# Kernel optimization log

Measured on AMD Instinct MI355X. Metric: run time of the kernel, lower is better.

## Reference

```python
import jax, jax.numpy as jnp
import numpy as np

DIM = 768  # N, feature length and Linear dim
B, C = 16, 1024  # batch, token count


def setup_inputs() -> dict:
    key = jax.random.key(0)
    ks = jax.random.split(key, 7)
    s = 1.0 / np.sqrt(DIM)
    return {
        "x": jax.random.normal(ks[0], (B, C, DIM), dtype=jnp.float32),
        "Wq": jax.random.uniform(ks[1], (DIM, DIM), jnp.float32, -s, s),
        "bq": jax.random.uniform(ks[2], (DIM,), jnp.float32, -s, s),
        "Wk": jax.random.uniform(ks[3], (DIM, DIM), jnp.float32, -s, s),
        "bk": jax.random.uniform(ks[4], (DIM,), jnp.float32, -s, s),
        "Wv": jax.random.uniform(ks[5], (DIM, DIM), jnp.float32, -s, s),
        "bv": jax.random.uniform(ks[6], (DIM,), jnp.float32, -s, s),
    }


def reference(x, Wq, bq, Wk, bk, Wv, bv):
    # x: [B, C, N] with N == DIM; Linears act on last axis (torch y = x W^T + b)
    Bb, Cc, N = x.shape
    q = jnp.einsum("bcn,dn->bcd", x, Wq) + bq
    k = jnp.einsum("bcn,dn->bcd", x, Wk) + bk
    v = jnp.einsum("bcn,dn->bcd", x, Wv) + bv
    attn = jax.nn.softmax(jnp.einsum("bcd,bed->bce", q, k) * (N ** -0.5), axis=-1)  # [B,C,C]
    out = jnp.einsum("bce,ben->bcn", attn, v)  # [B,C,N]
    # faithful to torch: transpose(1,2) then reshape back to (B,C,N) -- a buffer reinterpretation
    out = jnp.transpose(out, (0, 2, 1)).reshape(Bb, Cc, N)
    return out + x  # dropout is identity at inference
```

## Files before the change

kernel.cpp:

```cpp
#include <hip/hip_runtime.h>
#include <hip/hip_bf16.h>

typedef __bf16 v8bf __attribute__((ext_vector_type(8)));
typedef float f32x4 __attribute__((ext_vector_type(4)));

static __device__ __forceinline__ unsigned short f2b(float f){
  union { float f; unsigned int u; } c; c.f = f;
  return (unsigned short)((c.u + 0x7FFFu + ((c.u >> 16) & 1u)) >> 16);
}
static __device__ __forceinline__ float b2f(unsigned int h){
  union { unsigned int u; float f; } c; c.u = h << 16; return c.f;
}

static __device__ __forceinline__ void gld_lds16(const void* g, void* l){
  __builtin_amdgcn_global_load_lds(
      (const __attribute__((address_space(1))) unsigned int*)g,
      (__attribute__((address_space(3))) unsigned int*)l, 16, 0, 0);
}

#define FENCE __builtin_amdgcn_sched_barrier(0)

template<int NW>
static __device__ __forceinline__ void gemm2p(
    const unsigned short* __restrict__ A, int lda,
    const unsigned short* __restrict__ B, int ldb,
    int NT, unsigned short* smem, f32x4 acc[8][NW])
{
  const int tid  = threadIdx.x;
  const int lane = tid & 63;
  const int w    = tid >> 6;
  const int wr   = w >> 2, wc = w & 3;
  const int lr   = lane & 15, lg = lane >> 4;
  char* sm = (char*)smem;
  constexpr int BBUF = NW*8192;

  #pragma unroll
  for (int m=0;m<8;++m)
    #pragma unroll
    for (int n=0;n<NW;++n)
      acc[m][n] = (f32x4){0.f,0.f,0.f,0.f};

  const int rloc = tid >> 3;
  const int scol = ((tid & 7) ^ ((tid >> 3) & 7)) << 3;
  const unsigned short* Ab0 = A + (size_t)rloc*lda + scol;
  const unsigned short* Bb0 = B + (size_t)rloc*ldb + scol;

  auto stA = [&](int ab, int i, int kE){
    gld_lds16(Ab0 + (size_t)(i*64)*lda + kE, sm + ab*32768 + i*8192 + w*1024);
  };
  auto stB = [&](int db, int i, int kE){
    gld_lds16(Bb0 + (size_t)(i*64)*ldb + kE, sm + 98304 + db*BBUF + i*8192 + w*1024);
  };

  const int ce0 = (((lg*8))      ^ ((lr&7)<<3)) * 2;
  const int ce1 = (((32 + lg*8)) ^ ((lr&7)<<3)) * 2;

  v8bf aLo[4][2], aHi[4][2], bE[NW][2], bO[NW][2];

  auto rdAh = [&](v8bf (&dst)[4][2], int ab, int half){
    char* base = sm + ab*32768 + (wr*128 + half*64 + lr)*128;
    #pragma unroll
    for (int f=0; f<4; ++f){
      char* rp = base + f*2048;
      dst[f][0] = *(const v8bf*)(rp + ce0);
      dst[f][1] = *(const v8bf*)(rp + ce1);
    }
  };
  auto rdB = [&](v8bf (&dst)[NW][2], int db){
    char* base = sm + 98304 + db*BBUF + (wc*(NW*16) + lr)*128;
    #pragma unroll
    for (int n=0;n<NW;++n){
      char* rp = base + n*2048;
      dst[n][0] = *(const v8bf*)(rp + ce0);
      dst[n][1] = *(const v8bf*)(rp + ce1);
    }
  };

  auto tile = [&](int kt, v8bf (&bcur)[NW][2], v8bf (&bnext)[NW][2]){
    const int ab_r = kt % 3;
    const int ab_n = (ab_r==2) ? 0 : ab_r+1;
    const int ab_s = (ab_n==2) ? 0 : ab_n+1;
    const int db_r = kt & 1;
    const int kS = (kt+2 < NT ? kt+2 : NT-1)*64;

    stA(ab_s,0,kS); stA(ab_s,1,kS); stA(ab_s,2,kS); stA(ab_s,3,kS);
    rdAh(aHi, ab_r, 1);
    FENCE; asm volatile("s_waitcnt lgkmcnt(8)" ::: "memory"); FENCE;
    __builtin_amdgcn_s_setprio(1);
    #pragma unroll
    for (int f=0; f<4; ++f)
      #pragma unroll
      for (int n=0;n<NW;++n){
        acc[f][n] = __builtin_amdgcn_mfma_f32_16x16x32_bf16(aLo[f][0], bcur[n][0], acc[f][n], 0,0,0);
        acc[f][n] = __builtin_amdgcn_mfma_f32_16x16x32_bf16(aLo[f][1], bcur[n][1], acc[f][n], 0,0,0);
      }
    __builtin_amdgcn_s_setprio(0);
    asm volatile("s_waitcnt vmcnt(4)" ::: "memory");
    __builtin_amdgcn_s_barrier();

    #pragma unroll
    for (int i=0;i<NW;++i) stB(db_r, i, kS);
    rdAh(aLo, ab_n, 0);
    rdB(bnext, db_r^1);
    FENCE; asm volatile("s_waitcnt lgkmcnt(14)" ::: "memory"); FENCE;
    __builtin_amdgcn_s_setprio(1);
    #pragma unroll
    for (int f=0; f<4; ++f)
      #pragma unroll
      for (int n=0;n<NW;++n){
        acc[4+f][n] = __builtin_amdgcn_mfma_f32_16x16x32_bf16(aHi[f][0], bcur[n][0], acc[4+f][n], 0,0,0);
        acc[4+f][n] = __builtin_amdgcn_mfma_f32_16x16x32_bf16(aHi[f][1], bcur[n][1], acc[4+f][n], 0,0,0);
      }
    __builtin_amdgcn_s_setprio(0);
    __builtin_amdgcn_s_barrier();
  };

  #pragma unroll
  for (int i=0;i<4;++i)  stA(0,i,0);
  #pragma unroll
  for (int i=0;i<NW;++i) stB(0,i,0);
  #pragma unroll
  for (int i=0;i<4;++i)  stA(1,i,64);
  #pragma unroll
  for (int i=0;i<NW;++i) stB(1,i,64);
  asm volatile("s_waitcnt vmcnt(7)" ::: "memory");
  __builtin_amdgcn_s_barrier();
  rdAh(aLo, 0, 0);
  rdB(bE, 0);

  for (int kt = 0; kt < NT; kt += 2) {
    tile(kt,   bE, bO);
    tile(kt+1, bO, bE);
  }
}

static __device__ __forceinline__ void gemm256v1(
    const unsigned short* __restrict__ A, int lda,
    const unsigned short* __restrict__ B, int ldb,
    int NT, unsigned short* smem, f32x4 acc[8][4])
{
  const int tid  = threadIdx.x;
  const int lane = tid & 63;
  const int w    = tid >> 6;
  const int wr   = w >> 2, wc = w & 3;
  const int lr   = lane & 15, lg = lane >> 4;
  char* sm = (char*)smem;

  #pragma unroll
  for (int m=0;m<8;++m)
    #pragma unroll
    for (int n=0;n<4;++n)
      acc[m][n] = (f32x4){0.f,0.f,0.f,0.f};

  const int rloc = tid >> 3;
  const int scol = ((tid & 7) ^ ((tid >> 3) & 7)) << 3;
  const unsigned short* Ab0 = A + (size_t)rloc*lda + scol;
  const unsigned short* Bb0 = B + (size_t)rloc*ldb + scol;

  auto stA = [&](int ds, int i, int kE){
    gld_lds16(Ab0 + (size_t)(i*64)*lda + kE, sm + ds*32768 + i*8192 + w*1024);
  };
  auto stB = [&](int ds, int i, int kE){
    gld_lds16(Bb0 + (size_t)(i*64)*ldb + kE, sm + 65536 + ds*32768 + i*8192 + w*1024);
  };

  #pragma unroll
  for (int i=0;i<4;++i) stA(0,i,0);
  #pragma unroll
  for (int i=0;i<4;++i) stB(0,i,0);
  #pragma unroll
  for (int i=0;i<4;++i) stB(1,i,64);
  asm volatile("s_waitcnt vmcnt(4)" ::: "memory");
  __builtin_amdgcn_s_barrier();

  const int ce0 = (((lg*8))      ^ ((lr&7)<<3)) * 2;
  const int ce1 = (((32 + lg*8)) ^ ((lr&7)<<3)) * 2;

  for (int kt = 0; kt < NT; ++kt) {
    const int d  = kt & 1;
    char* Abase = sm + d*32768 + wr*16384;
    char* Bbase = sm + 65536 + d*32768 + wc*8192;
    const int kA = (kt+1 < NT ? kt+1 : NT-1)*64;
    const int kB = (kt+2 < NT ? kt+2 : NT-1)*64;
    v8bf bfr[4][2], af0[2][2], af1[2][2];

    auto rdA = [&](v8bf (&dst)[2][2], int qq){
      #pragma unroll
      for (int mm=0;mm<2;++mm){
        char* rp = Abase + ((qq*2+mm)*16+lr)*128;
        dst[mm][0] = *(const v8bf*)(rp + ce0);
        dst[mm][1] = *(const v8bf*)(rp + ce1);
      }
    };
    auto domfma = [&](v8bf (&cur)[2][2], int qq){
      #pragma unroll
      for (int mm=0;mm<2;++mm)
        #pragma unroll
        for (int n=0;n<4;++n){
          acc[qq*2+mm][n] = __builtin_amdgcn_mfma_f32_16x16x32_bf16(cur[mm][0], bfr[n][0], acc[qq*2+mm][n], 0,0,0);
          acc[qq*2+mm][n] = __builtin_amdgcn_mfma_f32_16x16x32_bf16(cur[mm][1], bfr[n][1], acc[qq*2+mm][n], 0,0,0);
        }
    };

    #pragma unroll
    for (int q=0;q<4;++q) {
      if (q==0) {
        #pragma unroll
        for (int n=0;n<4;++n){
          char* rp = Bbase + (n*16+lr)*128;
          bfr[n][0] = *(const v8bf*)(rp + ce0);
          bfr[n][1] = *(const v8bf*)(rp + ce1);
        }
        rdA(af0, 0);
      } else {
        if ((q&1)==0) rdA(af0, q); else rdA(af1, q);
      }
      if      (q==0){ stA(d^1,0,kA); stA(d^1,1,kA); }
      else if (q==1){ stA(d^1,2,kA); stA(d^1,3,kA); }
      else if (q==2){ stB(d,0,kB);   stB(d,1,kB);   }
      else          { stB(d,2,kB);   stB(d,3,kB);   }
      __builtin_amdgcn_s_barrier();
      asm volatile("s_waitcnt lgkmcnt(0)" ::: "memory");
      FENCE;
      __builtin_amdgcn_s_setprio(1);
      if ((q&1)==0) domfma(af0, q); else domfma(af1, q);
      __builtin_amdgcn_s_setprio(0);
      if (q==3) asm volatile("s_waitcnt vmcnt(4)" ::: "memory");
      __builtin_amdgcn_s_barrier();
    }
  }
}

__global__ __launch_bounds__(256) void convert_kernel(
    const float* __restrict__ x,
    const float* __restrict__ Wq, const float* __restrict__ Wk,
    const float* __restrict__ Wv,
    unsigned short* __restrict__ Xb, unsigned short* __restrict__ Wb)
{
  const int NX = 3145728;
  const int NW_ = 147456;
  const int total = NX + 3*NW_;
  for (int i = blockIdx.x*256 + threadIdx.x; i < total; i += gridDim.x*256) {
    const float* src; unsigned short* dst; int off;
    if (i < NX) { src = x; dst = Xb; off = i; }
    else {
      int j = i - NX; int z = j / NW_; off = j - z*NW_;
      src = (z==0) ? Wq : ((z==1) ? Wk : Wv);
      dst = Wb + (size_t)z*589824;
    }
    float4 v = reinterpret_cast<const float4*>(src)[off];
    ushort4 h; h.x=f2b(v.x); h.y=f2b(v.y); h.z=f2b(v.z); h.w=f2b(v.w);
    reinterpret_cast<ushort4*>(dst)[off] = h;
  }
}

__global__ __launch_bounds__(512, 2) void qkv_kernel(
    const unsigned short* __restrict__ Xb, const unsigned short* __restrict__ Wb,
    const float* __restrict__ bq, const float* __restrict__ bk,
    const float* __restrict__ bv,
    unsigned short* __restrict__ Qb, unsigned short* __restrict__ Kb,
    unsigned short* __restrict__ Vt)
{
  extern __shared__ unsigned short smem[];
  const int bid = blockIdx.x;
  const int wg  = (bid & 7)*96 + (bid >> 3);
  const int mt  = wg / 12, nt = wg % 12;

  f32x4 acc[8][3];
  gemm2p<3>(Xb + (size_t)mt*256*768, 768,
            Wb + (size_t)nt*192*768, 768, 12, smem, acc);

  const int tid = threadIdx.x, lane = tid & 63, w = tid >> 6;
  const int wr = w >> 2, wc = w & 3, lr = lane & 15, lg = lane >> 4;
  const int z = nt >> 2;
  const float* bias = (z==0) ? bq : ((z==1) ? bk : bv);
  const int colbase = (nt & 3)*192 + wc*48;

  if (z < 2) {
    unsigned short* dst = (z==0) ? Qb : Kb;
    #pragma unroll
    for (int m=0;m<8;++m){
      int row0 = mt*256 + wr*128 + m*16 + lg*4;
      #pragma unroll
      for (int n=0;n<3;++n){
        int col = colbase + n*16 + lr;
        float bb = bias[col];
        #pragma unroll
        for (int r=0;r<4;++r)
          dst[(size_t)(row0+r)*768 + col] = f2b(acc[m][n][r] + bb);
      }
    }
  } else {
    const int rowG0 = mt*256;
    const int batch = rowG0 >> 10;
    const int ebase = rowG0 & 1023;
    unsigned short* dst = Vt + (size_t)batch*786432;
    #pragma unroll
    for (int m=0;m<8;++m){
      int e0 = ebase + wr*128 + m*16 + lg*4;
      #pragma unroll
      for (int n=0;n<3;++n){
        int col = colbase + n*16 + lr;
        float bb = bias[col];
        ushort4 h;
        h.x = f2b(acc[m][n][0] + bb);
        h.y = f2b(acc[m][n][1] + bb);
        h.z = f2b(acc[m][n][2] + bb);
        h.w = f2b(acc[m][n][3] + bb);
        *reinterpret_cast<ushort4*>(dst + (size_t)col*1024 + e0) = h;
      }
    }
  }
}

__global__ __launch_bounds__(512, 2) void scores_kernel(
    const unsigned short* __restrict__ Qb,
    const unsigned short* __restrict__ Kb,
    unsigned short* __restrict__ Eb)
{
  extern __shared__ unsigned short smem[];
  const int mt = blockIdx.x, nt = blockIdx.y, b = blockIdx.z;

  f32x4 acc[8][4];
  gemm256v1(Qb + (size_t)b*786432 + (size_t)mt*256*768, 768,
            Kb + (size_t)b*786432 + (size_t)nt*256*768, 768, 12, smem, acc);

  const float scale = 0.03608439182435161f;
  const int tid = threadIdx.x, lane = tid & 63, w = tid >> 6;
  const int wr = w >> 2, wc = w & 3, lr = lane & 15, lg = lane >> 4;
  unsigned short* dst = Eb + (size_t)b*1048576;
  #pragma unroll
  for (int m=0;m<8;++m){
    int row0 = mt*256 + wr*128 + m*16 + lg*4;
    #pragma unroll
    for (int n=0;n<4;++n){
      int col = nt*256 + wc*64 + n*16 + lr;
      #pragma unroll
      for (int r=0;r<4;++r)
        dst[(size_t)(row0+r)*1024 + col] = f2b(__expf(acc[m][n][r] * scale));
    }
  }
}

__global__ __launch_bounds__(256) void rowsum_kernel(
    const unsigned short* __restrict__ E, float* __restrict__ D)
{
  int row  = blockIdx.x*4 + (threadIdx.x >> 6);
  int lane = threadIdx.x & 63;
  const unsigned short* p = E + (size_t)row*1024 + lane*16;
  uint4 v0 = *reinterpret_cast<const uint4*>(p);
  uint4 v1 = *reinterpret_cast<const uint4*>(p + 8);
  unsigned int uu[8] = {v0.x, v0.y, v0.z, v0.w, v1.x, v1.y, v1.z, v1.w};
  float s = 0.f;
  #pragma unroll
  for (int i=0;i<8;++i){ s += b2f(uu[i] & 0xffffu); s += b2f(uu[i] >> 16); }
  #pragma unroll
  for (int off=1; off<64; off<<=1) s += __shfl_xor(s, off, 64);
  if (lane == 0) D[row] = s;
}

__global__ __launch_bounds__(512, 2) void pv_kernel(
    const unsigned short* __restrict__ Eb,
    const unsigned short* __restrict__ Vt,
    const float* __restrict__ D,
    const float* __restrict__ x, float* __restrict__ out)
{
  extern __shared__ unsigned short smem[];
  const int mt = blockIdx.x, nt = blockIdx.y, b = blockIdx.z;

  f32x4 acc[8][3];
  gemm2p<3>(Eb + (size_t)b*1048576 + (size_t)mt*256*1024, 1024,
            Vt + (size_t)b*786432  + (size_t)nt*192*1024, 1024, 16, smem, acc);

  const int tid = threadIdx.x, lane = tid & 63, w = tid >> 6;
  const int wr = w >> 2, wc = w & 3, lr = lane & 15, lg = lane >> 4;
  const float* xb = x   + (size_t)b*786432;
  float*       ob = out + (size_t)b*786432;
  const float* Db = D + b*1024;
  #pragma unroll
  for (int m=0;m<8;++m){
    int c0 = mt*256 + wr*128 + m*16 + lg*4;
    float inv0 = 1.0f / Db[c0+0];
    float inv1 = 1.0f / Db[c0+1];
    float inv2 = 1.0f / Db[c0+2];
    float inv3 = 1.0f / Db[c0+3];
    #pragma unroll
    for (int n=0;n<3;++n){
      int col = nt*192 + wc*48 + n*16 + lr;
      size_t idx = (size_t)col*1024 + c0;
      float4 xv = *reinterpret_cast<const float4*>(xb + idx);
      float4 o;
      o.x = acc[m][n][0]*inv0 + xv.x;
      o.y = acc[m][n][1]*inv1 + xv.y;
      o.z = acc[m][n][2]*inv2 + xv.z;
      o.w = acc[m][n][3]*inv3 + xv.w;
      *reinterpret_cast<float4*>(ob + idx) = o;
    }
  }
}

extern "C" void kernel_launch(void* const* d_in, const int* in_sizes, int n_in,
                              void* d_out, int out_size, void* d_ws, size_t ws_size,
                              hipStream_t stream)
{
  const float* x  = (const float*)d_in[0];
  const float* Wq = (const float*)d_in[1];
  const float* bq = (const float*)d_in[2];
  const float* Wk = (const float*)d_in[3];
  const float* bk = (const float*)d_in[4];
  const float* Wv = (const float*)d_in[5];
  const float* bv = (const float*)d_in[6];
  float* out = (float*)d_out;

  char* ws = (char*)d_ws;
  unsigned short* Xb = (unsigned short*)(ws);
  unsigned short* Wb = (unsigned short*)(ws + 25165824);
  unsigned short* Eb = (unsigned short*)(ws);
  unsigned short* Qb = (unsigned short*)(ws + 33554432);
  float*          Dd = (float*)         (ws + 33554432);
  unsigned short* Kb = (unsigned short*)(ws + 58720256);
  unsigned short* Vt = (unsigned short*)(ws + 83886080);

  convert_kernel<<<dim3(2048),     dim3(256), 0,      stream>>>(x, Wq, Wk, Wv, Xb, Wb);
  qkv_kernel    <<<dim3(768),      dim3(512), 147456, stream>>>(Xb, Wb, bq, bk, bv, Qb, Kb, Vt);
  scores_kernel <<<dim3(4, 4, 16), dim3(512), 131072, stream>>>(Qb, Kb, Eb);
  rowsum_kernel <<<dim3(4096),     dim3(256), 0,      stream>>>(Eb, Dd);
  pv_kernel     <<<dim3(4, 4, 16), dim3(512), 147456, stream>>>(Eb, Vt, Dd, x, out);
}
```

Baseline: 162.7 us.

## Shrink QKV and PV GEMM tiles to 128x192 with simple double buffering

Replaces the 256x192 triple/double-buffered split-phase GEMM core with a smaller 128x192 tile that uses a plain double-buffered loop and full waitcnt barriers. This cuts LDS per block to 80 KB and doubles the grid for the QKV and PV kernels, with launch bounds raised for more resident blocks, to improve occupancy and CU fill. In exchange, each tile reuses data less, the loop keeps less load/compute overlap (vmcnt(0) and lgkmcnt(0) each iteration), and global traffic rises. The scores GEMM is only renamed.

```diff
diff --git a/kernel.cpp b/kernel.cpp
--- a/kernel.cpp
+++ b/kernel.cpp
@@ -20,11 +20,10 @@
 
 #define FENCE __builtin_amdgcn_sched_barrier(0)
 
-template<int NW>
-static __device__ __forceinline__ void gemm2p(
+static __device__ __forceinline__ void gemm128(
     const unsigned short* __restrict__ A, int lda,
     const unsigned short* __restrict__ B, int ldb,
-    int NT, unsigned short* smem, f32x4 acc[8][NW])
+    int NT, unsigned short* smem, f32x4 acc[4][3])
 {
   const int tid  = threadIdx.x;
   const int lane = tid & 63;
@@ -32,12 +31,11 @@
   const int wr   = w >> 2, wc = w & 3;
   const int lr   = lane & 15, lg = lane >> 4;
   char* sm = (char*)smem;
-  constexpr int BBUF = NW*8192;
-
-  #pragma unroll
-  for (int m=0;m<8;++m)
-    #pragma unroll
-    for (int n=0;n<NW;++n)
+
+  #pragma unroll
+  for (int m=0;m<4;++m)
+    #pragma unroll
+    for (int n=0;n<3;++n)
       acc[m][n] = (f32x4){0.f,0.f,0.f,0.f};
 
   const int rloc = tid >> 3;
@@ -45,96 +43,57 @@
   const unsigned short* Ab0 = A + (size_t)rloc*lda + scol;
   const unsigned short* Bb0 = B + (size_t)rloc*ldb + scol;
 
-  auto stA = [&](int ab, int i, int kE){
-    gld_lds16(Ab0 + (size_t)(i*64)*lda + kE, sm + ab*32768 + i*8192 + w*1024);
+  auto stA = [&](int d, int i, int kE){
+    gld_lds16(Ab0 + (size_t)(i*64)*lda + kE, sm + d*16384 + i*8192 + w*1024);
   };
-  auto stB = [&](int db, int i, int kE){
-    gld_lds16(Bb0 + (size_t)(i*64)*ldb + kE, sm + 98304 + db*BBUF + i*8192 + w*1024);
+  auto stB = [&](int d, int i, int kE){
+    gld_lds16(Bb0 + (size_t)(i*64)*ldb + kE, sm + 32768 + d*24576 + i*8192 + w*1024);
   };
 
   const int ce0 = (((lg*8))      ^ ((lr&7)<<3)) * 2;
   const int ce1 = (((32 + lg*8)) ^ ((lr&7)<<3)) * 2;
 
-  v8bf aLo[4][2], aHi[4][2], bE[NW][2], bO[NW][2];
-
-  auto rdAh = [&](v8bf (&dst)[4][2], int ab, int half){
-    char* base = sm + ab*32768 + (wr*128 + half*64 + lr)*128;
-    #pragma unroll
-    for (int f=0; f<4; ++f){
-      char* rp = base + f*2048;
-      dst[f][0] = *(const v8bf*)(rp + ce0);
-      dst[f][1] = *(const v8bf*)(rp + ce1);
-    }
-  };
-  auto rdB = [&](v8bf (&dst)[NW][2], int db){
-    char* base = sm + 98304 + db*BBUF + (wc*(NW*16) + lr)*128;
-    #pragma unroll
-    for (int n=0;n<NW;++n){
-      char* rp = base + n*2048;
-      dst[n][0] = *(const v8bf*)(rp + ce0);
-      dst[n][1] = *(const v8bf*)(rp + ce1);
-    }
-  };
-
-  auto tile = [&](int kt, v8bf (&bcur)[NW][2], v8bf (&bnext)[NW][2]){
-    const int ab_r = kt % 3;
-    const int ab_n = (ab_r==2) ? 0 : ab_r+1;
-    const int ab_s = (ab_n==2) ? 0 : ab_n+1;
-    const int db_r = kt & 1;
-    const int kS = (kt+2 < NT ? kt+2 : NT-1)*64;
-
-    stA(ab_s,0,kS); stA(ab_s,1,kS); stA(ab_s,2,kS); stA(ab_s,3,kS);
-    rdAh(aHi, ab_r, 1);
-    FENCE; asm volatile("s_waitcnt lgkmcnt(8)" ::: "memory"); FENCE;
+  stA(0,0,0); stA(0,1,0);
+  stB(0,0,0); stB(0,1,0); stB(0,2,0);
+  asm volatile("s_waitcnt vmcnt(0)" ::: "memory");
+  __builtin_amdgcn_s_barrier();
+
+  for (int kt = 0; kt < NT; ++kt) {
+    const int d  = kt & 1;
+    const int kN = (kt+1 < NT ? kt+1 : NT-1)*64;
+    stA(d^1,0,kN); stA(d^1,1,kN);
+    stB(d^1,0,kN); stB(d^1,1,kN); stB(d^1,2,kN);
+    v8bf a[4][2], b[3][2];
+    char* Abase = sm + d*16384;
+    char* Bbase = sm + 32768 + d*24576;
+    #pragma unroll
+    for (int m=0;m<4;++m){
+      char* rp = Abase + (wr*64 + m*16 + lr)*128;
+      a[m][0] = *(const v8bf*)(rp + ce0);
+      a[m][1] = *(const v8bf*)(rp + ce1);
+    }
+    #pragma unroll
+    for (int n=0;n<3;++n){
+      char* rp = Bbase + (wc*48 + n*16 + lr)*128;
+      b[n][0] = *(const v8bf*)(rp + ce0);
+      b[n][1] = *(const v8bf*)(rp + ce1);
+    }
+    FENCE; asm volatile("s_waitcnt lgkmcnt(0)" ::: "memory"); FENCE;
     __builtin_amdgcn_s_setprio(1);
     #pragma unroll
-    for (int f=0; f<4; ++f)
-      #pragma unroll
-      for (int n=0;n<NW;++n){
-        acc[f][n] = __builtin_amdgcn_mfma_f32_16x16x32_bf16(aLo[f][0], bcur[n][0], acc[f][n], 0,0,0);
-        acc[f][n] = __builtin_amdgcn_mfma_f32_16x16x32_bf16(aLo[f][1], bcur[n][1], acc[f][n], 0,0,0);
+    for (int m=0;m<4;++m)
+      #pragma unroll
+      for (int n=0;n<3;++n){
+        acc[m][n] = __builtin_amdgcn_mfma_f32_16x16x32_bf16(a[m][0], b[n][0], acc[m][n], 0,0,0);
+        acc[m][n] = __builtin_amdgcn_mfma_f32_16x16x32_bf16(a[m][1], b[n][1], acc[m][n], 0,0,0);
       }
     __builtin_amdgcn_s_setprio(0);
-    asm volatile("s_waitcnt vmcnt(4)" ::: "memory");
+    asm volatile("s_waitcnt vmcnt(0)" ::: "memory");
     __builtin_amdgcn_s_barrier();
-
-    #pragma unroll
-    for (int i=0;i<NW;++i) stB(db_r, i, kS);
-    rdAh(aLo, ab_n, 0);
-    rdB(bnext, db_r^1);
-    FENCE; asm volatile("s_waitcnt lgkmcnt(14)" ::: "memory"); FENCE;
-    __builtin_amdgcn_s_setprio(1);
-    #pragma unroll
-    for (int f=0; f<4; ++f)
-      #pragma unroll
-      for (int n=0;n<NW;++n){
-        acc[4+f][n] = __builtin_amdgcn_mfma_f32_16x16x32_bf16(aHi[f][0], bcur[n][0], acc[4+f][n], 0,0,0);
-        acc[4+f][n] = __builtin_amdgcn_mfma_f32_16x16x32_bf16(aHi[f][1], bcur[n][1], acc[4+f][n], 0,0,0);
-      }
-    __builtin_amdgcn_s_setprio(0);
-    __builtin_amdgcn_s_barrier();
-  };
-
-  #pragma unroll
-  for (int i=0;i<4;++i)  stA(0,i,0);
-  #pragma unroll
-  for (int i=0;i<NW;++i) stB(0,i,0);
-  #pragma unroll
-  for (int i=0;i<4;++i)  stA(1,i,64);
-  #pragma unroll
-  for (int i=0;i<NW;++i) stB(1,i,64);
-  asm volatile("s_waitcnt vmcnt(7)" ::: "memory");
-  __builtin_amdgcn_s_barrier();
-  rdAh(aLo, 0, 0);
-  rdB(bE, 0);
-
-  for (int kt = 0; kt < NT; kt += 2) {
-    tile(kt,   bE, bO);
-    tile(kt+1, bO, bE);
-  }
-}
-
-static __device__ __forceinline__ void gemm256v1(
+  }
+}
+
+static __device__ __forceinline__ void gemmcore4(
     const unsigned short* __restrict__ A, int lda,
     const unsigned short* __restrict__ B, int ldb,
     int NT, unsigned short* smem, f32x4 acc[8][4])
@@ -254,7 +213,7 @@
   }
 }
 
-__global__ __launch_bounds__(512, 2) void qkv_kernel(
+__global__ __launch_bounds__(512, 4) void qkv_kernel(
     const unsigned short* __restrict__ Xb, const unsigned short* __restrict__ Wb,
     const float* __restrict__ bq, const float* __restrict__ bk,
     const float* __restrict__ bv,
@@ -263,12 +222,12 @@
 {
   extern __shared__ unsigned short smem[];
   const int bid = blockIdx.x;
-  const int wg  = (bid & 7)*96 + (bid >> 3);
+  const int wg  = (bid & 7)*192 + (bid >> 3);
   const int mt  = wg / 12, nt = wg % 12;
 
-  f32x4 acc[8][3];
-  gemm2p<3>(Xb + (size_t)mt*256*768, 768,
-            Wb + (size_t)nt*192*768, 768, 12, smem, acc);
+  f32x4 acc[4][3];
+  gemm128(Xb + (size_t)mt*128*768, 768,
+          Wb + (size_t)nt*192*768, 768, 12, smem, acc);
 
   const int tid = threadIdx.x, lane = tid & 63, w = tid >> 6;
   const int wr = w >> 2, wc = w & 3, lr = lane & 15, lg = lane >> 4;
@@ -279,8 +238,8 @@
   if (z < 2) {
     unsigned short* dst = (z==0) ? Qb : Kb;
     #pragma unroll
-    for (int m=0;m<8;++m){
-      int row0 = mt*256 + wr*128 + m*16 + lg*4;
+    for (int m=0;m<4;++m){
+      int row0 = mt*128 + wr*64 + m*16 + lg*4;
       #pragma unroll
       for (int n=0;n<3;++n){
         int col = colbase + n*16 + lr;
@@ -291,13 +250,12 @@
       }
     }
   } else {
-    const int rowG0 = mt*256;
-    const int batch = rowG0 >> 10;
-    const int ebase = rowG0 & 1023;
+    const int batch = mt >> 3;
+    const int ebase = (mt & 7)*128;
     unsigned short* dst = Vt + (size_t)batch*786432;
     #pragma unroll
-    for (int m=0;m<8;++m){
-      int e0 = ebase + wr*128 + m*16 + lg*4;
+    for (int m=0;m<4;++m){
+      int e0 = ebase + wr*64 + m*16 + lg*4;
       #pragma unroll
       for (int n=0;n<3;++n){
         int col = colbase + n*16 + lr;
@@ -322,8 +280,9 @@
   const int mt = blockIdx.x, nt = blockIdx.y, b = blockIdx.z;
 
   f32x4 acc[8][4];
-  gemm256v1(Qb + (size_t)b*786432 + (size_t)mt*256*768, 768,
-            Kb + (size_t)b*786432 + (size_t)nt*256*768, 768, 12, smem, acc);
+  gemmcore4(Qb + (size_t)b*786432 + (size_t)mt*256*768, 768,
+            Kb + (size_t)b*786432 + (size_t)nt*256*768, 768,
+            12, smem, acc);
 
   const float scale = 0.03608439182435161f;
   const int tid = threadIdx.x, lane = tid & 63, w = tid >> 6;
@@ -359,7 +318,7 @@
   if (lane == 0) D[row] = s;
 }
 
-__global__ __launch_bounds__(512, 2) void pv_kernel(
+__global__ __launch_bounds__(512, 4) void pv_kernel(
     const unsigned short* __restrict__ Eb,
     const unsigned short* __restrict__ Vt,
     const float* __restrict__ D,
@@ -368,9 +327,10 @@
   extern __shared__ unsigned short smem[];
   const int mt = blockIdx.x, nt = blockIdx.y, b = blockIdx.z;
 
-  f32x4 acc[8][3];
-  gemm2p<3>(Eb + (size_t)b*1048576 + (size_t)mt*256*1024, 1024,
-            Vt + (size_t)b*786432  + (size_t)nt*192*1024, 1024, 16, smem, acc);
+  f32x4 acc[4][3];
+  gemm128(Eb + (size_t)b*1048576 + (size_t)mt*128*1024, 1024,
+          Vt + (size_t)b*786432  + (size_t)nt*192*1024, 1024,
+          16, smem, acc);
 
   const int tid = threadIdx.x, lane = tid & 63, w = tid >> 6;
   const int wr = w >> 2, wc = w & 3, lr = lane & 15, lg = lane >> 4;
@@ -378,8 +338,8 @@
   float*       ob = out + (size_t)b*786432;
   const float* Db = D + b*1024;
   #pragma unroll
-  for (int m=0;m<8;++m){
-    int c0 = mt*256 + wr*128 + m*16 + lg*4;
+  for (int m=0;m<4;++m){
+    int c0 = mt*128 + wr*64 + m*16 + lg*4;
     float inv0 = 1.0f / Db[c0+0];
     float inv1 = 1.0f / Db[c0+1];
     float inv2 = 1.0f / Db[c0+2];
@@ -422,8 +382,8 @@
   unsigned short* Vt = (unsigned short*)(ws + 83886080);
 
   convert_kernel<<<dim3(2048),     dim3(256), 0,      stream>>>(x, Wq, Wk, Wv, Xb, Wb);
-  qkv_kernel    <<<dim3(768),      dim3(512), 147456, stream>>>(Xb, Wb, bq, bk, bv, Qb, Kb, Vt);
+  qkv_kernel    <<<dim3(1536),     dim3(512), 81920,  stream>>>(Xb, Wb, bq, bk, bv, Qb, Kb, Vt);
   scores_kernel <<<dim3(4, 4, 16), dim3(512), 131072, stream>>>(Qb, Kb, Eb);
   rowsum_kernel <<<dim3(4096),     dim3(256), 0,      stream>>>(Eb, Dd);
-  pv_kernel     <<<dim3(4, 4, 16), dim3(512), 147456, stream>>>(Eb, Vt, Dd, x, out);
-}
+  pv_kernel     <<<dim3(8, 4, 16), dim3(512), 81920,  stream>>>(Eb, Vt, Dd, x, out);
+}
```

After: 161.8 us. Within noise of the previous version (-0.5%).
